# Optimization experiments

Measured on AMD Instinct MI355X. Metric: run time of the kernel, lower is better.

The kernel has to match this reference:

```python
import jax, jax.numpy as jnp
import numpy as np

N_NODES = 50000
N_EDGES = 800000
IN_DIM = 96
NUM_HEADS = 8
HEAD_DIM = IN_DIM // NUM_HEADS  # 12


def setup_inputs() -> dict:
    key = jax.random.key(0)
    ks = jax.random.split(key, 11)
    s = 1.0 / np.sqrt(IN_DIM)
    return {
        "x": jax.random.normal(ks[0], (N_NODES, IN_DIM), dtype=jnp.float32),
        "edge_index": jax.random.randint(ks[1], (2, N_EDGES), 0, N_NODES, dtype=jnp.int64),
        "edge_attr": jax.random.normal(ks[2], (N_EDGES, IN_DIM), dtype=jnp.float32),
        # Linear weights stored as [in, out] (apply as x @ W + b)
        "Wq": jax.random.normal(ks[3], (IN_DIM, IN_DIM), dtype=jnp.float32) * s,
        "bq": jax.random.normal(ks[4], (IN_DIM,), dtype=jnp.float32) * s,
        "Wk": jax.random.normal(ks[5], (IN_DIM, IN_DIM), dtype=jnp.float32) * s,
        "bk": jax.random.normal(ks[6], (IN_DIM,), dtype=jnp.float32) * s,
        "We": jax.random.normal(ks[7], (IN_DIM, IN_DIM), dtype=jnp.float32) * s,
        "be": jax.random.normal(ks[8], (IN_DIM,), dtype=jnp.float32) * s,
        "Wv": jax.random.normal(ks[9], (IN_DIM, IN_DIM), dtype=jnp.float32) * s,
        "bv": jax.random.normal(ks[10], (IN_DIM,), dtype=jnp.float32) * s,
    }


def reference(x, edge_index, edge_attr, Wq, bq, Wk, bk, We, be, Wv, bv):
    N = x.shape[0]
    H, D = NUM_HEADS, HEAD_DIM
    Q_h = (x @ Wq + bq).reshape(N, H, D)
    K_h = (x @ Wk + bk).reshape(N, H, D)
    V_h = (x @ Wv + bv).reshape(N, H, D)
    E = (edge_attr @ We + be).reshape(-1, H, D)

    src_idx = edge_index[0]
    dst_idx = edge_index[1]
    src = K_h[src_idx]               # [E, H, D]
    dest = Q_h[dst_idx]              # [E, H, D]
    score = (src * dest) / jnp.sqrt(jnp.asarray(D, x.dtype))
    score = score * E
    score = jnp.exp(jnp.clip(score.sum(-1, keepdims=True), -5.0, 5.0))  # [E, H, 1]

    msg = V_h[src_idx] * score       # [E, H, D]
    wV = jax.ops.segment_sum(msg, dst_idx, num_segments=N)      # [N, H, D]
    Z = jax.ops.segment_sum(score, dst_idx, num_segments=N)     # [N, H, 1]
    h_out = wV / (Z + 1e-6)
    return h_out.reshape(N, H * D)
```

## Files before the change

kernel.cpp:

```cpp
#include <hip/hip_runtime.h>
#include <math.h>

#define N_NODES 50000
#define N_EDGES 800000
#define IN_DIM 96
#define NHEADS 8
#define HDIM 12

#define QKV_BLOCKS 782
#define HIST_BLOCKS 3125
#define SCAN_BLOCKS 196
#define TPB 10
#define SCORE_GRID 1250

typedef __attribute__((ext_vector_type(8))) short short8;
typedef __attribute__((ext_vector_type(4))) float f32x4;

__device__ __forceinline__ unsigned short f2bf(float f) {
    unsigned int u = __float_as_uint(f);
    return (unsigned short)((u + 0x7FFFu + ((u >> 16) & 1u)) >> 16);
}
__device__ __forceinline__ float bf2f_lo(unsigned int u) {
    return __uint_as_float(u << 16);
}
__device__ __forceinline__ float bf2f_hi(unsigned int u) {
    return __uint_as_float(u & 0xFFFF0000u);
}
__device__ __forceinline__ unsigned int pack2(float a, float b) {
    return (unsigned int)f2bf(a) | ((unsigned int)f2bf(b) << 16);
}
__device__ __forceinline__ short8 pack8(const float4 lo, const float4 hi) {
    union { uint4 u; short8 s; } c;
    c.u.x = pack2(lo.x, lo.y);
    c.u.y = pack2(lo.z, lo.w);
    c.u.z = pack2(hi.x, hi.y);
    c.u.w = pack2(hi.z, hi.w);
    return c.s;
}

__global__ __launch_bounds__(256) void wet4_kernel(
    const float* __restrict__ Wq, const float* __restrict__ Wk,
    const float* __restrict__ Wv, const float* __restrict__ We,
    unsigned short* __restrict__ WqT, unsigned short* __restrict__ WkT,
    unsigned short* __restrict__ WvT, unsigned short* __restrict__ WeT)
{
    const int j = blockIdx.x * 256 + threadIdx.x;
    if (j >= 4 * 9216) return;
    const int m = j / 9216, r = j % 9216;
    const float* W = (m == 0) ? Wq : (m == 1) ? Wk : (m == 2) ? Wv : We;
    unsigned short* WT = (m == 0) ? WqT : (m == 1) ? WkT : (m == 2) ? WvT : WeT;
    const int k = r / 96, c = r % 96;
    WT[c * 96 + k] = f2bf(W[r]);
}

__global__ __launch_bounds__(256) void prep_kernel(
    const float* __restrict__ x,
    const float* __restrict__ bq, const float* __restrict__ bk,
    const float* __restrict__ bv,
    const unsigned short* __restrict__ WqT, const unsigned short* __restrict__ WkT,
    const unsigned short* __restrict__ WvT,
    const int* __restrict__ ei,
    unsigned short* __restrict__ Qb, unsigned short* __restrict__ Kb,
    unsigned short* __restrict__ Vb,
    int* __restrict__ cursor)
{
    const int t = threadIdx.x;
    const int bid = blockIdx.x;

    if (bid >= QKV_BLOCKS) {
        const int e = (bid - QKV_BLOCKS) * 256 + t;
        if (e < N_EDGES) atomicAdd(&cursor[ei[N_EDGES + e]], 1);
        return;
    }

    const int wid = t >> 6;
    const int lid = t & 63;
    const int l15 = lid & 15;
    const int lg  = lid >> 4;
    const int nbase = bid * 64 + wid * 16;

    int arow = nbase + l15;
    if (arow >= N_NODES) arow = N_NODES - 1;
    const float* xr = &x[(size_t)arow * 96 + lg * 8];
    short8 af[3];
    af[0] = pack8(*(const float4*)(xr + 0),  *(const float4*)(xr + 4));
    af[1] = pack8(*(const float4*)(xr + 32), *(const float4*)(xr + 36));
    af[2] = pack8(*(const float4*)(xr + 64), *(const float4*)(xr + 68));

    #pragma unroll
    for (int m = 0; m < 3; ++m) {
        const unsigned short* WT = (m == 0) ? WqT : (m == 1) ? WkT : WvT;
        const float* bias_p      = (m == 0) ? bq  : (m == 1) ? bk  : bv;
        unsigned short* Ob       = (m == 0) ? Qb  : (m == 1) ? Kb  : Vb;

        f32x4 acc[6] = {};
        #pragma unroll
        for (int kk = 0; kk < 3; ++kk) {
            #pragma unroll
            for (int ct = 0; ct < 6; ++ct) {
                const short8 b = *(const short8*)&WT[(ct * 16 + l15) * 96 + kk * 32 + lg * 8];
                acc[ct] = __builtin_amdgcn_mfma_f32_16x16x32_bf16(af[kk], b, acc[ct], 0, 0, 0);
            }
        }
        #pragma unroll
        for (int ct = 0; ct < 6; ++ct) {
            const int col = ct * 16 + l15;
            const float bias = bias_p[col];
            #pragma unroll
            for (int r = 0; r < 4; ++r) {
                const int n = nbase + lg * 4 + r;
                if (n < N_NODES)
                    Ob[(size_t)n * 96 + col] = f2bf(acc[ct][r] + bias);
            }
        }
    }
}

__global__ __launch_bounds__(256) void scanA_kernel(
    const int* __restrict__ cursor, int* __restrict__ partial)
{
    __shared__ int lds[256];
    const int t = threadIdx.x;
    const int idx = blockIdx.x * 256 + t;
    lds[t] = (idx < N_NODES) ? cursor[idx] : 0;
    __syncthreads();
    for (int off = 128; off > 0; off >>= 1) {
        if (t < off) lds[t] += lds[t + off];
        __syncthreads();
    }
    if (t == 0) partial[blockIdx.x] = lds[0];
}

__global__ __launch_bounds__(256) void scanB_kernel(
    int* __restrict__ partial, int* __restrict__ offsets)
{
    __shared__ int lds[256];
    const int t = threadIdx.x;
    const int v = (t < SCAN_BLOCKS) ? partial[t] : 0;
    lds[t] = v;
    __syncthreads();
    for (int off = 1; off < 256; off <<= 1) {
        const int u = (t >= off) ? lds[t - off] : 0;
        __syncthreads();
        lds[t] += u;
        __syncthreads();
    }
    if (t < SCAN_BLOCKS) partial[t] = lds[t] - v;
    if (t == 0) offsets[N_NODES] = N_EDGES;
}

__global__ __launch_bounds__(256) void scanC_kernel(
    int* __restrict__ cursor, const int* __restrict__ partial,
    int* __restrict__ offsets)
{
    __shared__ int lds[256];
    const int t = threadIdx.x;
    const int idx = blockIdx.x * 256 + t;
    const int v = (idx < N_NODES) ? cursor[idx] : 0;
    lds[t] = v;
    __syncthreads();
    for (int off = 1; off < 256; off <<= 1) {
        const int u = (t >= off) ? lds[t - off] : 0;
        __syncthreads();
        lds[t] += u;
        __syncthreads();
    }
    const int excl = lds[t] - v + partial[blockIdx.x];
    if (idx < N_NODES) {
        offsets[idx] = excl;
        cursor[idx] = excl;
    }
}

__global__ __launch_bounds__(256, 2) void score_kernel(
    const float* __restrict__ ea,
    const int* __restrict__ ei,
    const unsigned short* __restrict__ WeT,
    const float* __restrict__ be,
    const unsigned short* __restrict__ Qb, const unsigned short* __restrict__ Kb,
    int* __restrict__ cursor,
    int* __restrict__ sorted_src,
    float* __restrict__ score_s)
{
    __shared__ unsigned short WsT[96 * 104];
    __shared__ unsigned short epb[4][16 * 104];
    __shared__ float bes[96];

    const int t = threadIdx.x;
    const int wid = t >> 6;
    const int lid = t & 63;
    const int l15 = lid & 15;
    const int lg  = lid >> 4;
    const int er  = lid >> 3;
    const int h   = lid & 7;
    unsigned short* myep = epb[wid];
    const long t0 = (long)blockIdx.x * TPB;

#define LOAD_EI(V, TILE) do { \
    const long wb_ = (long)(TILE) * 64 + wid * 16; \
    (V) = 0; \
    if (lid < 32) (V) = (lid < 16) ? ei[wb_ + lid] : ei[N_EDGES + wb_ + (lid - 16)]; \
} while (0)

#define LOAD_EA(EA, TILE) do { \
    const float* ar_ = &ea[((long)(TILE) * 64 + wid * 16 + l15) * 96 + lg * 8]; \
    (EA)[0] = *(const float4*)(ar_ + 0);  (EA)[1] = *(const float4*)(ar_ + 4); \
    (EA)[2] = *(const float4*)(ar_ + 32); (EA)[3] = *(const float4*)(ar_ + 36); \
    (EA)[4] = *(const float4*)(ar_ + 64); (EA)[5] = *(const float4*)(ar_ + 68); \
} while (0)

#define ISSUE_GATHER(V, KQ, P0, P1) do { \
    const int s0_ = __shfl((V), er, 64); \
    const int d0_ = __shfl((V), 16 + er, 64); \
    const int s1_ = __shfl((V), 8 + er, 64); \
    const int d1_ = __shfl((V), 24 + er, 64); \
    const uint2* K0_ = (const uint2*)&Kb[(size_t)s0_ * 96 + h * 12]; \
    const uint2* Q0_ = (const uint2*)&Qb[(size_t)d0_ * 96 + h * 12]; \
    const uint2* K1_ = (const uint2*)&Kb[(size_t)s1_ * 96 + h * 12]; \
    const uint2* Q1_ = (const uint2*)&Qb[(size_t)d1_ * 96 + h * 12]; \
    (KQ)[0] = K0_[0]; (KQ)[1] = K0_[1]; (KQ)[2] = K0_[2]; \
    (KQ)[3] = Q0_[0]; (KQ)[4] = Q0_[1]; (KQ)[5] = Q0_[2]; \
    (KQ)[6] = K1_[0]; (KQ)[7] = K1_[1]; (KQ)[8] = K1_[2]; \
    (KQ)[9] = Q1_[0]; (KQ)[10] = Q1_[1]; (KQ)[11] = Q1_[2]; \
    const int md_ = __shfl((V), 16 + l15, 64); \
    int pv_ = 0; \
    if (lid < 16) { pv_ = atomicAdd(&cursor[md_], 1); sorted_src[pv_] = (V); } \
    (P0) = __shfl(pv_, er, 64); \
    (P1) = __shfl(pv_, 8 + er, 64); \
} while (0)

#define MFMA_EPB(EA) do { \
    const short8 af0_ = pack8((EA)[0], (EA)[1]); \
    const short8 af1_ = pack8((EA)[2], (EA)[3]); \
    const short8 af2_ = pack8((EA)[4], (EA)[5]); \
    f32x4 acc_[6] = {}; \
    _Pragma("unroll") \
    for (int ct = 0; ct < 6; ++ct) { \
        acc_[ct] = __builtin_amdgcn_mfma_f32_16x16x32_bf16(af0_, \
            *(const short8*)&WsT[(ct * 16 + l15) * 104 + 0 + lg * 8], acc_[ct], 0, 0, 0); \
        acc_[ct] = __builtin_amdgcn_mfma_f32_16x16x32_bf16(af1_, \
            *(const short8*)&WsT[(ct * 16 + l15) * 104 + 32 + lg * 8], acc_[ct], 0, 0, 0); \
        acc_[ct] = __builtin_amdgcn_mfma_f32_16x16x32_bf16(af2_, \
            *(const short8*)&WsT[(ct * 16 + l15) * 104 + 64 + lg * 8], acc_[ct], 0, 0, 0); \
    } \
    _Pragma("unroll") \
    for (int ct = 0; ct < 6; ++ct) { \
        const int col_ = ct * 16 + l15; \
        const float b_ = bes[col_]; \
        _Pragma("unroll") \
        for (int r = 0; r < 4; ++r) \
            myep[(lg * 4 + r) * 104 + col_] = f2bf(acc_[ct][r] + b_); \
    } \
} while (0)

#define ACC3(KU, QU, EU) \
    s_ += bf2f_lo(KU) * bf2f_lo(QU) * bf2f_lo(EU) + \
          bf2f_hi(KU) * bf2f_hi(QU) * bf2f_hi(EU);

#define SCORE_PHASE(KQ, P0, P1) do { \
    _Pragma("unroll") \
    for (int pass_ = 0; pass_ < 2; ++pass_) { \
        const int rl_ = pass_ * 8 + er; \
        const int pos_ = pass_ ? (P1) : (P0); \
        const unsigned short* ep_ = &myep[rl_ * 104 + h * 12]; \
        const uint2 u0_ = *(const uint2*)&ep_[0]; \
        const uint2 u1_ = *(const uint2*)&ep_[4]; \
        const uint2 u2_ = *(const uint2*)&ep_[8]; \
        const uint2 ka_ = (KQ)[pass_ * 6 + 0]; \
        const uint2 kb_ = (KQ)[pass_ * 6 + 1]; \
        const uint2 kc_ = (KQ)[pass_ * 6 + 2]; \
        const uint2 qa_ = (KQ)[pass_ * 6 + 3]; \
        const uint2 qb_ = (KQ)[pass_ * 6 + 4]; \
        const uint2 qc_ = (KQ)[pass_ * 6 + 5]; \
        float s_ = 0.f; \
        ACC3(ka_.x, qa_.x, u0_.x); ACC3(ka_.y, qa_.y, u0_.y); \
        ACC3(kb_.x, qb_.x, u1_.x); ACC3(kb_.y, qb_.y, u1_.y); \
        ACC3(kc_.x, qc_.x, u2_.x); ACC3(kc_.y, qc_.y, u2_.y); \
        s_ *= 0.2886751345948129f; \
        s_ = fminf(fmaxf(s_, -5.f), 5.f); \
        score_s[(size_t)pos_ * 8 + h] = __expf(s_); \
    } \
} while (0)

    int vA, vB;
    float4 eaA[6], eaB[6];
    uint2 kqA[12], kqB[12];
    int pA0 = 0, pA1 = 0, pB0 = 0, pB1 = 0;

    LOAD_EI(vA, t0);
    LOAD_EA(eaA, t0);
    LOAD_EI(vB, t0 + 1);
    LOAD_EA(eaB, t0 + 1);

    for (int j = t; j < 96 * 12; j += 256) {
        const int c = j / 12, kc = j % 12;
        *(uint4*)&WsT[c * 104 + kc * 8] = *(const uint4*)&WeT[c * 96 + kc * 8];
    }
    if (t < 96) bes[t] = be[t];
    __syncthreads();

    ISSUE_GATHER(vA, kqA, pA0, pA1);

    #pragma unroll 1
    for (int i = 0; i < TPB; i += 2) {
        MFMA_EPB(eaA);
        ISSUE_GATHER(vB, kqB, pB0, pB1);
        if (i + 2 < TPB) { LOAD_EI(vA, t0 + i + 2); LOAD_EA(eaA, t0 + i + 2); }
        SCORE_PHASE(kqA, pA0, pA1);

        MFMA_EPB(eaB);
        if (i + 2 < TPB) ISSUE_GATHER(vA, kqA, pA0, pA1);
        if (i + 3 < TPB) { LOAD_EI(vB, t0 + i + 3); LOAD_EA(eaB, t0 + i + 3); }
        SCORE_PHASE(kqB, pB0, pB1);
    }

#undef LOAD_EI
#undef LOAD_EA
#undef ISSUE_GATHER
#undef MFMA_EPB
#undef ACC3
#undef SCORE_PHASE
}

__global__ __launch_bounds__(256) void gather_kernel(
    const int* __restrict__ offsets, const int* __restrict__ sorted_src,
    const float* __restrict__ score_s, const unsigned short* __restrict__ Vb,
    float* __restrict__ out)
{
    const int gid = blockIdx.x * 256 + threadIdx.x;
    if (gid >= N_NODES * 4) return;
    const int n = gid >> 2;
    const int g = gid & 3;

    const int s0 = offsets[n];
    const int s1 = offsets[n + 1];

    float acc[24];
    #pragma unroll
    for (int i = 0; i < 24; ++i) acc[i] = 0.f;
    float z0 = 0.f, z1 = 0.f;

#define ACCUM(U0, U1, U2, SC) \
    acc[0]  += SC.x * bf2f_lo(U0.x); acc[1]  += SC.x * bf2f_hi(U0.x); \
    acc[2]  += SC.x * bf2f_lo(U0.y); acc[3]  += SC.x * bf2f_hi(U0.y); \
    acc[4]  += SC.x * bf2f_lo(U0.z); acc[5]  += SC.x * bf2f_hi(U0.z); \
    acc[6]  += SC.x * bf2f_lo(U0.w); acc[7]  += SC.x * bf2f_hi(U0.w); \
    acc[8]  += SC.x * bf2f_lo(U1.x); acc[9]  += SC.x * bf2f_hi(U1.x); \
    acc[10] += SC.x * bf2f_lo(U1.y); acc[11] += SC.x * bf2f_hi(U1.y); \
    acc[12] += SC.y * bf2f_lo(U1.z); acc[13] += SC.y * bf2f_hi(U1.z); \
    acc[14] += SC.y * bf2f_lo(U1.w); acc[15] += SC.y * bf2f_hi(U1.w); \
    acc[16] += SC.y * bf2f_lo(U2.x); acc[17] += SC.y * bf2f_hi(U2.x); \
    acc[18] += SC.y * bf2f_lo(U2.y); acc[19] += SC.y * bf2f_hi(U2.y); \
    acc[20] += SC.y * bf2f_lo(U2.z); acc[21] += SC.y * bf2f_hi(U2.z); \
    acc[22] += SC.y * bf2f_lo(U2.w); acc[23] += SC.y * bf2f_hi(U2.w);

    int p = s0;
    for (; p + 2 <= s1; p += 2) {
        const int srcA = sorted_src[p];
        const int srcB = sorted_src[p + 1];
        const float2 scA = *(const float2*)&score_s[(size_t)p * 8 + g * 2];
        const float2 scB = *(const float2*)&score_s[(size_t)(p + 1) * 8 + g * 2];
        const uint4* VA = (const uint4*)&Vb[(size_t)srcA * 96 + g * 24];
        const uint4* VB = (const uint4*)&Vb[(size_t)srcB * 96 + g * 24];
        const uint4 a0 = VA[0], a1 = VA[1], a2 = VA[2];
        const uint4 b0 = VB[0], b1 = VB[1], b2 = VB[2];
        ACCUM(a0, a1, a2, scA);
        ACCUM(b0, b1, b2, scB);
        z0 += scA.x + scB.x;
        z1 += scA.y + scB.y;
    }
    if (p < s1) {
        const int srcA = sorted_src[p];
        const float2 scA = *(const float2*)&score_s[(size_t)p * 8 + g * 2];
        const uint4* VA = (const uint4*)&Vb[(size_t)srcA * 96 + g * 24];
        const uint4 a0 = VA[0], a1 = VA[1], a2 = VA[2];
        ACCUM(a0, a1, a2, scA);
        z0 += scA.x;
        z1 += scA.y;
    }
#undef ACCUM

    const float i0 = 1.f / (z0 + 1e-6f);
    const float i1 = 1.f / (z1 + 1e-6f);
    float o[24];
    #pragma unroll
    for (int k = 0; k < 24; ++k) o[k] = acc[k] * (k < 12 ? i0 : i1);
    float* dst = &out[(size_t)n * 96 + g * 24];
    #pragma unroll
    for (int k = 0; k < 6; ++k)
        *(float4*)&dst[k * 4] = make_float4(o[k*4], o[k*4+1], o[k*4+2], o[k*4+3]);
}

extern "C" void kernel_launch(void* const* d_in, const int* in_sizes, int n_in,
                              void* d_out, int out_size, void* d_ws, size_t ws_size,
                              hipStream_t stream) {
    const float* x  = (const float*)d_in[0];
    const int*   ei = (const int*)d_in[1];
    const float* ea = (const float*)d_in[2];
    const float* Wq = (const float*)d_in[3];
    const float* bq = (const float*)d_in[4];
    const float* Wk = (const float*)d_in[5];
    const float* bk = (const float*)d_in[6];
    const float* We = (const float*)d_in[7];
    const float* be = (const float*)d_in[8];
    const float* Wv = (const float*)d_in[9];
    const float* bv = (const float*)d_in[10];

    float* out = (float*)d_out;

    const size_t nqkv = (size_t)N_NODES * 96;
    unsigned short* Qb = (unsigned short*)d_ws;
    unsigned short* Kb = Qb + nqkv;
    unsigned short* Vb = Kb + nqkv;
    float* score_s  = (float*)(Vb + nqkv);
    int* offsets    = (int*)(score_s + (size_t)N_EDGES * 8);
    int* cursor     = offsets + (N_NODES + 1);
    int* sorted_src = cursor + N_NODES;
    unsigned short* WeT = (unsigned short*)(sorted_src + N_EDGES);
    unsigned short* WqT = WeT + 9216;
    unsigned short* WkT = WqT + 9216;
    unsigned short* WvT = WkT + 9216;
    int* partial = (int*)(WvT + 9216);

    hipMemsetAsync(cursor, 0, N_NODES * sizeof(int), stream);

    wet4_kernel<<<dim3(144), 256, 0, stream>>>(
        Wq, Wk, Wv, We, WqT, WkT, WvT, WeT);

    prep_kernel<<<dim3(QKV_BLOCKS + HIST_BLOCKS), 256, 0, stream>>>(
        x, bq, bk, bv, WqT, WkT, WvT, ei, Qb, Kb, Vb, cursor);

    scanA_kernel<<<dim3(SCAN_BLOCKS), 256, 0, stream>>>(cursor, partial);
    scanB_kernel<<<dim3(1), 256, 0, stream>>>(partial, offsets);
    scanC_kernel<<<dim3(SCAN_BLOCKS), 256, 0, stream>>>(cursor, partial, offsets);

    score_kernel<<<dim3(SCORE_GRID), 256, 0, stream>>>(
        ea, ei, WeT, be, Qb, Kb, cursor, sorted_src, score_s);

    gather_kernel<<<dim3((N_NODES * 4 + 255) / 256), 256, 0, stream>>>(
        offsets, sorted_src, score_s, Vb, out);
}
```

Measured before the change: 239.1 us.

## Store edge scores as bf16 and deepen gather prefetch in score kernel

Edge scores are written by the score kernel and read by the gather kernel as bf16 instead of fp32, halving that intermediate traffic. The score loop is restructured so K/Q gathers are issued one stage earlier and edge indices are prefetched two tiles ahead, overlapping more gather latency with MFMA work. Launch bounds are raised to three blocks per CU. The risks are reduced score precision in the normalized output and register pressure from the tighter occupancy bound, which could cause spills.

```diff
diff --git a/kernel.cpp b/kernel.cpp
--- a/kernel.cpp
+++ b/kernel.cpp
@@ -172,7 +172,7 @@
     }
 }
 
-__global__ __launch_bounds__(256, 2) void score_kernel(
+__global__ __launch_bounds__(256, 3) void score_kernel(
     const float* __restrict__ ea,
     const int* __restrict__ ei,
     const unsigned short* __restrict__ WeT,
@@ -180,7 +180,7 @@
     const unsigned short* __restrict__ Qb, const unsigned short* __restrict__ Kb,
     int* __restrict__ cursor,
     int* __restrict__ sorted_src,
-    float* __restrict__ score_s)
+    unsigned short* __restrict__ score_b)
 {
     __shared__ unsigned short WsT[96 * 104];
     __shared__ unsigned short epb[4][16 * 104];
@@ -278,7 +278,7 @@
         ACC3(kc_.x, qc_.x, u2_.x); ACC3(kc_.y, qc_.y, u2_.y); \
         s_ *= 0.2886751345948129f; \
         s_ = fminf(fmaxf(s_, -5.f), 5.f); \
-        score_s[(size_t)pos_ * 8 + h] = __expf(s_); \
+        score_b[(size_t)pos_ * 8 + h] = f2bf(__expf(s_)); \
     } \
 } while (0)
 
@@ -288,8 +288,8 @@
     int pA0 = 0, pA1 = 0, pB0 = 0, pB1 = 0;
 
     LOAD_EI(vA, t0);
+    LOAD_EI(vB, t0 + 1);
     LOAD_EA(eaA, t0);
-    LOAD_EI(vB, t0 + 1);
     LOAD_EA(eaB, t0 + 1);
 
     for (int j = t; j < 96 * 12; j += 256) {
@@ -300,18 +300,27 @@
     __syncthreads();
 
     ISSUE_GATHER(vA, kqA, pA0, pA1);
+    ISSUE_GATHER(vB, kqB, pB0, pB1);
+    LOAD_EI(vA, t0 + 2);
+    LOAD_EI(vB, t0 + 3);
 
     #pragma unroll 1
     for (int i = 0; i < TPB; i += 2) {
         MFMA_EPB(eaA);
-        ISSUE_GATHER(vB, kqB, pB0, pB1);
-        if (i + 2 < TPB) { LOAD_EI(vA, t0 + i + 2); LOAD_EA(eaA, t0 + i + 2); }
         SCORE_PHASE(kqA, pA0, pA1);
+        if (i + 2 < TPB) {
+            ISSUE_GATHER(vA, kqA, pA0, pA1);
+            LOAD_EA(eaA, t0 + i + 2);
+        }
+        if (i + 4 < TPB) LOAD_EI(vA, t0 + i + 4);
 
         MFMA_EPB(eaB);
-        if (i + 2 < TPB) ISSUE_GATHER(vA, kqA, pA0, pA1);
-        if (i + 3 < TPB) { LOAD_EI(vB, t0 + i + 3); LOAD_EA(eaB, t0 + i + 3); }
         SCORE_PHASE(kqB, pB0, pB1);
+        if (i + 3 < TPB) {
+            ISSUE_GATHER(vB, kqB, pB0, pB1);
+            LOAD_EA(eaB, t0 + i + 3);
+        }
+        if (i + 5 < TPB) LOAD_EI(vB, t0 + i + 5);
     }
 
 #undef LOAD_EI
@@ -324,7 +333,7 @@
 
 __global__ __launch_bounds__(256) void gather_kernel(
     const int* __restrict__ offsets, const int* __restrict__ sorted_src,
-    const float* __restrict__ score_s, const unsigned short* __restrict__ Vb,
+    const unsigned short* __restrict__ score_b, const unsigned short* __restrict__ Vb,
     float* __restrict__ out)
 {
     const int gid = blockIdx.x * 256 + threadIdx.x;
@@ -340,43 +349,46 @@
     for (int i = 0; i < 24; ++i) acc[i] = 0.f;
     float z0 = 0.f, z1 = 0.f;
 
-#define ACCUM(U0, U1, U2, SC) \
-    acc[0]  += SC.x * bf2f_lo(U0.x); acc[1]  += SC.x * bf2f_hi(U0.x); \
-    acc[2]  += SC.x * bf2f_lo(U0.y); acc[3]  += SC.x * bf2f_hi(U0.y); \
-    acc[4]  += SC.x * bf2f_lo(U0.z); acc[5]  += SC.x * bf2f_hi(U0.z); \
-    acc[6]  += SC.x * bf2f_lo(U0.w); acc[7]  += SC.x * bf2f_hi(U0.w); \
-    acc[8]  += SC.x * bf2f_lo(U1.x); acc[9]  += SC.x * bf2f_hi(U1.x); \
-    acc[10] += SC.x * bf2f_lo(U1.y); acc[11] += SC.x * bf2f_hi(U1.y); \
-    acc[12] += SC.y * bf2f_lo(U1.z); acc[13] += SC.y * bf2f_hi(U1.z); \
-    acc[14] += SC.y * bf2f_lo(U1.w); acc[15] += SC.y * bf2f_hi(U1.w); \
-    acc[16] += SC.y * bf2f_lo(U2.x); acc[17] += SC.y * bf2f_hi(U2.x); \
-    acc[18] += SC.y * bf2f_lo(U2.y); acc[19] += SC.y * bf2f_hi(U2.y); \
-    acc[20] += SC.y * bf2f_lo(U2.z); acc[21] += SC.y * bf2f_hi(U2.z); \
-    acc[22] += SC.y * bf2f_lo(U2.w); acc[23] += SC.y * bf2f_hi(U2.w);
+#define ACCUM(U0, U1, U2, SX, SY) \
+    acc[0]  += SX * bf2f_lo(U0.x); acc[1]  += SX * bf2f_hi(U0.x); \
+    acc[2]  += SX * bf2f_lo(U0.y); acc[3]  += SX * bf2f_hi(U0.y); \
+    acc[4]  += SX * bf2f_lo(U0.z); acc[5]  += SX * bf2f_hi(U0.z); \
+    acc[6]  += SX * bf2f_lo(U0.w); acc[7]  += SX * bf2f_hi(U0.w); \
+    acc[8]  += SX * bf2f_lo(U1.x); acc[9]  += SX * bf2f_hi(U1.x); \
+    acc[10] += SX * bf2f_lo(U1.y); acc[11] += SX * bf2f_hi(U1.y); \
+    acc[12] += SY * bf2f_lo(U1.z); acc[13] += SY * bf2f_hi(U1.z); \
+    acc[14] += SY * bf2f_lo(U1.w); acc[15] += SY * bf2f_hi(U1.w); \
+    acc[16] += SY * bf2f_lo(U2.x); acc[17] += SY * bf2f_hi(U2.x); \
+    acc[18] += SY * bf2f_lo(U2.y); acc[19] += SY * bf2f_hi(U2.y); \
+    acc[20] += SY * bf2f_lo(U2.z); acc[21] += SY * bf2f_hi(U2.z); \
+    acc[22] += SY * bf2f_lo(U2.w); acc[23] += SY * bf2f_hi(U2.w);
 
     int p = s0;
     for (; p + 2 <= s1; p += 2) {
         const int srcA = sorted_src[p];
         const int srcB = sorted_src[p + 1];
-        const float2 scA = *(const float2*)&score_s[(size_t)p * 8 + g * 2];
-        const float2 scB = *(const float2*)&score_s[(size_t)(p + 1) * 8 + g * 2];
+        const unsigned int sA = *(const unsigned int*)&score_b[(size_t)p * 8 + g * 2];
+        const unsigned int sB = *(const unsigned int*)&score_b[(size_t)(p + 1) * 8 + g * 2];
+        const float sAx = bf2f_lo(sA), sAy = bf2f_hi(sA);
+        const float sBx = bf2f_lo(sB), sBy = bf2f_hi(sB);
         const uint4* VA = (const uint4*)&Vb[(size_t)srcA * 96 + g * 24];
         const uint4* VB = (const uint4*)&Vb[(size_t)srcB * 96 + g * 24];
         const uint4 a0 = VA[0], a1 = VA[1], a2 = VA[2];
         const uint4 b0 = VB[0], b1 = VB[1], b2 = VB[2];
-        ACCUM(a0, a1, a2, scA);
-        ACCUM(b0, b1, b2, scB);
-        z0 += scA.x + scB.x;
-        z1 += scA.y + scB.y;
+        ACCUM(a0, a1, a2, sAx, sAy);
+        ACCUM(b0, b1, b2, sBx, sBy);
+        z0 += sAx + sBx;
+        z1 += sAy + sBy;
     }
     if (p < s1) {
         const int srcA = sorted_src[p];
-        const float2 scA = *(const float2*)&score_s[(size_t)p * 8 + g * 2];
+        const unsigned int sA = *(const unsigned int*)&score_b[(size_t)p * 8 + g * 2];
+        const float sAx = bf2f_lo(sA), sAy = bf2f_hi(sA);
         const uint4* VA = (const uint4*)&Vb[(size_t)srcA * 96 + g * 24];
         const uint4 a0 = VA[0], a1 = VA[1], a2 = VA[2];
-        ACCUM(a0, a1, a2, scA);
-        z0 += scA.x;
-        z1 += scA.y;
+        ACCUM(a0, a1, a2, sAx, sAy);
+        z0 += sAx;
+        z1 += sAy;
     }
 #undef ACCUM
 
@@ -412,8 +424,8 @@
     unsigned short* Qb = (unsigned short*)d_ws;
     unsigned short* Kb = Qb + nqkv;
     unsigned short* Vb = Kb + nqkv;
-    float* score_s  = (float*)(Vb + nqkv);
-    int* offsets    = (int*)(score_s + (size_t)N_EDGES * 8);
+    unsigned short* score_b = Vb + nqkv;
+    int* offsets    = (int*)(score_b + (size_t)N_EDGES * 8);
     int* cursor     = offsets + (N_NODES + 1);
     int* sorted_src = cursor + N_NODES;
     unsigned short* WeT = (unsigned short*)(sorted_src + N_EDGES);
@@ -435,8 +447,8 @@
     scanC_kernel<<<dim3(SCAN_BLOCKS), 256, 0, stream>>>(cursor, partial, offsets);
 
     score_kernel<<<dim3(SCORE_GRID), 256, 0, stream>>>(
-        ea, ei, WeT, be, Qb, Kb, cursor, sorted_src, score_s);
+        ea, ei, WeT, be, Qb, Kb, cursor, sorted_src, score_b);
 
     gather_kernel<<<dim3((N_NODES * 4 + 255) / 256), 256, 0, stream>>>(
-        offsets, sorted_src, score_s, Vb, out);
-}
+        offsets, sorted_src, score_b, Vb, out);
+}
```

Measured after the change: 242.4 us. About the same (+1.4%).
